# Optimization experiments

Hardware: AMD Instinct MI355X
Metric: run time of the kernel (lower is better)

## Reference

```python
import jax, jax.numpy as jnp
import numpy as np

N = 25000      # nodes
E = 400000     # edges (before self-loops)
D = 64         # input node feature dim
H = 4          # attention heads
C = 64         # out channels per head (concat=False -> head mean)
L = 3          # stacked layers
NEG_SLOPE = 0.2
EPS = 1e-5


def setup_inputs() -> dict:
    key = jax.random.key(0)
    ks = jax.random.split(key, 8)
    s = 0.1
    return {
        "x": jax.random.normal(ks[0], (N, D), jnp.float32),
        "edge_index": jax.random.randint(ks[1], (2, E), 0, N, dtype=jnp.int64),
        "Wl": jax.random.normal(ks[2], (L, H * C, D), jnp.float32) * s,
        "bl": jnp.zeros((L, H * C), jnp.float32),
        "Wr": jax.random.normal(ks[3], (L, H * C, D), jnp.float32) * s,
        "br": jnp.zeros((L, H * C), jnp.float32),
        "att": jax.random.normal(ks[4], (L, H, C), jnp.float32) * s,
        "conv_bias": jnp.zeros((L, C), jnp.float32),
        "gn_weight": jnp.ones((L, C), jnp.float32),
        "gn_scale": jnp.ones((L, C), jnp.float32),   # GraphNorm mean_scale (alpha)
        "gn_bias": jnp.zeros((L, C), jnp.float32),
    }


def _gat_forward(x, src, dst, Wl, bl, Wr, br, att, conv_bias,
                 gn_weight, gn_scale, gn_bias):
    n = x.shape[0]
    for i in range(L):
        # GATv2Conv (edge_attr=None, concat=False): separate source/target projections
        xl = (x @ Wl[i].T + bl[i]).reshape(n, H, C)  # [N,H,C]
        xr = (x @ Wr[i].T + br[i]).reshape(n, H, C)
        # per-edge attention logits: att . leaky_relu(xl[j] + xr[i])
        e = jax.nn.leaky_relu(xl[src] + xr[dst], NEG_SLOPE)      # [E',H,C]
        logits = jnp.einsum('ehc,hc->eh', e, att[i])             # [E',H]
        # segment softmax over incoming edges of each target node
        m = jax.ops.segment_max(logits, dst, num_segments=n)     # [N,H]
        a = jnp.exp(logits - m[dst])
        denom = jax.ops.segment_sum(a, dst, num_segments=n)      # [N,H]
        alpha = a / denom[dst]                                   # [E',H]
        # weighted scatter-add of source messages, mean over heads
        agg = jax.ops.segment_sum(xl[src] * alpha[:, :, None], dst,
                                  num_segments=n)                # [N,H,C]
        h = agg.mean(axis=1) + conv_bias[i]                      # [N,C]
        # GraphNorm (single graph): x - alpha*mean, scale by rstd
        mu = h.mean(axis=0)
        hc = h - gn_scale[i] * mu
        var = jnp.mean(hc * hc, axis=0)
        x = hc * jax.lax.rsqrt(var + EPS) * gn_weight[i] + gn_bias[i]
        # Dropout p=0 at eval -> identity
    return x


def reference(x, edge_index, Wl, bl, Wr, br, att, conv_bias,
              gn_weight, gn_scale, gn_bias):
    n = x.shape[0]
    loop = jnp.arange(n, dtype=edge_index.dtype)
    # PyG GATv2Conv adds self-loops by default
    src = jnp.concatenate([edge_index[0], loop])
    dst = jnp.concatenate([edge_index[1], loop])
    return _gat_forward(x, src, dst, Wl, bl, Wr, br, att, conv_bias,
                        gn_weight, gn_scale, gn_bias)
```

## Files before the change

### kernel.cpp

```cpp
#include <hip/hip_runtime.h>
#include <hip/hip_fp16.h>
#include <math.h>

#define HC   256
#define DD   64
#define CC   64
#define NLAY 3

#define RCAP    64
#define RCAP_SH 6

typedef _Float16 h2 __attribute__((ext_vector_type(2)));
typedef _Float16 h4 __attribute__((ext_vector_type(4)));
typedef _Float16 h8 __attribute__((ext_vector_type(8)));
typedef float    f4 __attribute__((ext_vector_type(4)));
typedef float    f2 __attribute__((ext_vector_type(2)));

#define XSTR 72
#define OSTR 276

__global__ __launch_bounds__(256) void zero_kernel(int* __restrict__ counts,
                                                   float* __restrict__ stats,
                                                   int n) {
    int i = blockIdx.x * 256 + threadIdx.x;
    if (i < n) counts[i] = 0;
    if (i < NLAY * 128) stats[i] = 0.f;
}

__global__ __launch_bounds__(256) void fill_kernel(const int* __restrict__ srcArr,
                                                   const int* __restrict__ dstArr,
                                                   int* __restrict__ counts,
                                                   int* __restrict__ csr_src,
                                                   int e, int n) {
    int i = blockIdx.x * 256 + threadIdx.x;
    if (i >= e + n) return;
    int s, d;
    if (i < e) { s = srcArr[i]; d = dstArr[i]; }
    else       { s = d = i - e; }
    int slot = atomicAdd(&counts[d], 1);
    if (slot < RCAP) csr_src[(d << RCAP_SH) + slot] = s;
}

__global__ __launch_bounds__(256) void proj_kernel(const float* __restrict__ x,
                                                   const float* __restrict__ Wl,
                                                   const float* __restrict__ bl,
                                                   const float* __restrict__ Wr,
                                                   const float* __restrict__ br,
                                                   __half* __restrict__ xl,
                                                   __half* __restrict__ xr, int n,
                                                   const float* __restrict__ stats,
                                                   const float* __restrict__ pgw,
                                                   const float* __restrict__ pgs,
                                                   const float* __restrict__ pgb) {
    __shared__ _Float16 xs[64 * XSTR];
    __shared__ _Float16 ws[256 * XSTR];
    __shared__ float nrm_a[64], nrm_b[64];
    const int t  = threadIdx.x;
    const int n0 = blockIdx.x * 64;

    if (t < 64) {
        float a = 1.f, b = 0.f;
        if (stats) {
            float inv_n = 1.0f / (float)n;
            float mu  = stats[t] * inv_n;
            float eh2 = stats[64 + t] * inv_n;
            float al  = pgs[t];
            float var = eh2 - 2.f * al * mu * mu + al * al * mu * mu;
            float rstd = rsqrtf(var + 1e-5f);
            a = pgw[t] * rstd;
            b = pgb[t] - al * mu * a;
        }
        nrm_a[t] = a; nrm_b[t] = b;
    }
    __syncthreads();

    {
        const float* xb = x + (size_t)n0 * DD;
        const int limit = (n - n0) * DD;
        #pragma unroll
        for (int it = 0; it < 4; ++it) {
            int f = (it * 256 + t) * 4;
            float4 v = make_float4(0.f, 0.f, 0.f, 0.f);
            if (f + 3 < limit) v = *(const float4*)(xb + f);
            else {
                float tmp[4] = {0.f, 0.f, 0.f, 0.f};
                for (int q = 0; q < 4; ++q) if (f + q < limit) tmp[q] = xb[f + q];
                v = make_float4(tmp[0], tmp[1], tmp[2], tmp[3]);
            }
            int d = f & 63;
            const float4 a4 = *(const float4*)&nrm_a[d];
            const float4 b4 = *(const float4*)&nrm_b[d];
            h4 hv;
            hv.x = (_Float16)fmaf(v.x, a4.x, b4.x);
            hv.y = (_Float16)fmaf(v.y, a4.y, b4.y);
            hv.z = (_Float16)fmaf(v.z, a4.z, b4.z);
            hv.w = (_Float16)fmaf(v.w, a4.w, b4.w);
            *(h4*)&xs[(f >> 6) * XSTR + d] = hv;
        }
    }

    const int w = t >> 6, lane = t & 63, m = lane & 15, q = lane >> 4;

    h8 A0, A1;
    f4 acc[16];

    #define STAGE_W(Wsel)                                                     \
    {                                                                         \
        _Pragma("unroll")                                                     \
        for (int it = 0; it < 16; ++it) {                                     \
            int f = (it * 256 + t) * 4;                                       \
            float4 v = *(const float4*)((Wsel) + f);                          \
            h4 hv = { (_Float16)v.x, (_Float16)v.y, (_Float16)v.z,            \
                      (_Float16)v.w };                                        \
            *(h4*)&ws[(f >> 6) * XSTR + (f & 63)] = hv;                       \
        }                                                                     \
    }

    #define MFMA_PASS()                                                       \
    {                                                                         \
        _Pragma("unroll")                                                     \
        for (int ct = 0; ct < 16; ++ct) {                                     \
            const _Float16* brow = ws + (ct * 16 + m) * XSTR + q * 8;         \
            const h8 B0 = *(const h8*)brow;                                   \
            const h8 B1 = *(const h8*)(brow + 32);                            \
            f4 c = {0.f, 0.f, 0.f, 0.f};                                      \
            c = __builtin_amdgcn_mfma_f32_16x16x32_f16(A0, B0, c, 0, 0, 0);   \
            c = __builtin_amdgcn_mfma_f32_16x16x32_f16(A1, B1, c, 0, 0, 0);   \
            acc[ct] = c;                                                      \
        }                                                                     \
    }

    #define EPILOGUE(bsel, osel)                                              \
    {                                                                         \
        _Pragma("unroll")                                                     \
        for (int ct = 0; ct < 16; ++ct) {                                     \
            int ch = ct * 16 + m;                                             \
            float bv = (bsel)[ch];                                            \
            _Pragma("unroll")                                                 \
            for (int r = 0; r < 4; ++r)                                       \
                ws[(w * 16 + q * 4 + r) * OSTR + ch] =                        \
                    (_Float16)(acc[ct][r] + bv);                              \
        }                                                                     \
        __syncthreads();                                                      \
        _Pragma("unroll")                                                     \
        for (int it = 0; it < 8; ++it) {                                      \
            int f   = (it * 256 + t) * 8;                                     \
            int row = f >> 8, ch = f & 255;                                   \
            if (n0 + row < n)                                                 \
                *(uint4*)((osel) + (size_t)(n0 + row) * HC + ch) =            \
                    *(const uint4*)&ws[row * OSTR + ch];                      \
        }                                                                     \
    }

    STAGE_W(Wl)
    __syncthreads();
    {
        const _Float16* arow = xs + (w * 16 + m) * XSTR + q * 8;
        A0 = *(const h8*)arow;
        A1 = *(const h8*)(arow + 32);
    }
    MFMA_PASS()
    __syncthreads();
    EPILOGUE(bl, xl)
    __syncthreads();

    STAGE_W(Wr)
    __syncthreads();
    MFMA_PASS()
    __syncthreads();
    EPILOGUE(br, xr)

    #undef STAGE_W
    #undef MFMA_PASS
    #undef EPILOGUE
}

__global__ __launch_bounds__(256) void attn_kernel(const __half* __restrict__ xl,
                                                   const __half* __restrict__ xr,
                                                   const float* __restrict__ att,
                                                   const float* __restrict__ conv_bias,
                                                   const int* __restrict__ counts,
                                                   const int* __restrict__ csr_src,
                                                   float* __restrict__ h_out, int n) {
    const int wave = threadIdx.x >> 6;
    const int l    = threadIdx.x & 63;
    const int v    = blockIdx.x * 4 + wave;
    if (v >= n) return;

    const int e2 = l >> 5;
    const int h  = (l >> 3) & 3;
    const int co = l & 7;
    const int choff = h * CC + co * 8;

    h2 xr2[4];
    *(uint4*)xr2 = *(const uint4*)(xr + (size_t)v * HC + choff);
    h2 at2[4];
    {
        const float* ap = att + choff;
        float4 a0 = *(const float4*)(ap);
        float4 a1 = *(const float4*)(ap + 4);
        at2[0] = (h2){(_Float16)a0.x, (_Float16)a0.y};
        at2[1] = (h2){(_Float16)a0.z, (_Float16)a0.w};
        at2[2] = (h2){(_Float16)a1.x, (_Float16)a1.y};
        at2[3] = (h2){(_Float16)a1.z, (_Float16)a1.w};
    }
    const _Float16 k02 = (_Float16)0.2f;

    const int rs = v << RCAP_SH;
    const int re = rs + counts[v];

    float s = 0.f;
    h2 acch[4];
    #pragma unroll
    for (int q = 0; q < 4; ++q) acch[q] = (h2){(_Float16)0.f, (_Float16)0.f};

    #define CLAMPI(i) (((i) < re) ? (i) : rs)

    uint4 r0 = *(const uint4*)(xl + (size_t)csr_src[CLAMPI(rs + e2)]     * HC + choff);
    uint4 r1 = *(const uint4*)(xl + (size_t)csr_src[CLAMPI(rs + 2 + e2)] * HC + choff);
    uint4 r2 = *(const uint4*)(xl + (size_t)csr_src[CLAMPI(rs + 4 + e2)] * HC + choff);
    int jnA = csr_src[CLAMPI(rs + 6 + e2)];
    int jnB = csr_src[CLAMPI(rs + 8 + e2)];
    int jnC = csr_src[CLAMPI(rs + 10 + e2)];

    #define STAGE(RBUF, JREG, VOFF, JOFF)                                 \
    {                                                                     \
        const uint4 cur = RBUF;                                           \
        RBUF = *(const uint4*)(xl + (size_t)JREG * HC + choff);           \
        JREG = csr_src[CLAMPI(k + JOFF + e2)];                            \
        const bool valid = (k + VOFF + e2) < re;                          \
        const h2* xh = (const h2*)&cur;                                   \
        h2 d2 = (h2){(_Float16)0.f, (_Float16)0.f};                      \
        _Pragma("unroll")                                                 \
        for (int q = 0; q < 4; ++q) {                                     \
            h2 tt = xh[q] + xr2[q];                                       \
            h2 lk = __builtin_elementwise_max(tt, tt * k02);              \
            d2 += lk * at2[q];                                            \
        }                                                                 \
        float p = (float)d2.x + (float)d2.y;                              \
        p += __shfl_xor(p, 1, 64);                                        \
        p += __shfl_xor(p, 2, 64);                                        \
        p += __shfl_xor(p, 4, 64);                                        \
        float pe = valid ? __expf(p) : 0.f;                               \
        s += pe;                                                          \
        const _Float16 peh = (_Float16)pe;                                \
        const h2 pe2 = (h2){peh, peh};                                    \
        _Pragma("unroll")                                                 \
        for (int q = 0; q < 4; ++q)                                       \
            acch[q] += pe2 * xh[q];                                       \
    }

    for (int k = rs; k < re; k += 6) {
        STAGE(r0, jnA, 0, 12)
        STAGE(r1, jnB, 2, 14)
        STAGE(r2, jnC, 4, 16)
    }
    #undef STAGE
    #undef CLAMPI

    s += __shfl_xor(s, 32, 64);
    const float inv = 1.f / s;
    float out8[8];
    #pragma unroll
    for (int q = 0; q < 8; ++q) {
        float av = (q & 1) ? (float)acch[q >> 1].y : (float)acch[q >> 1].x;
        float a = av + __shfl_xor(av, 32, 64);
        a *= inv;
        a += __shfl_xor(a, 8, 64);
        a += __shfl_xor(a, 16, 64);
        out8[q] = 0.25f * a;
    }
    if (l < 8) {
        const float4 cb0 = *(const float4*)(conv_bias + co * 8);
        const float4 cb1 = *(const float4*)(conv_bias + co * 8 + 4);
        float4 o0 = make_float4(out8[0] + cb0.x, out8[1] + cb0.y,
                                out8[2] + cb0.z, out8[3] + cb0.w);
        float4 o1 = make_float4(out8[4] + cb1.x, out8[5] + cb1.y,
                                out8[6] + cb1.z, out8[7] + cb1.w);
        float* op = h_out + (size_t)v * CC + co * 8;
        *(float4*)op       = o0;
        *(float4*)(op + 4) = o1;
    }
}

__global__ __launch_bounds__(256) void stats_kernel(const float* __restrict__ h,
                                                    float* __restrict__ stats, int n) {
    int t = threadIdx.x;
    int c = t & 63, r = t >> 6;
    float s = 0.f, s2 = 0.f;
    for (int node = blockIdx.x * 4 + r; node < n; node += gridDim.x * 4) {
        float v = h[node * CC + c];
        s += v; s2 += v * v;
    }
    __shared__ float l1[256], l2[256];
    l1[t] = s; l2[t] = s2;
    __syncthreads();
    if (t < 64) {
        s  = l1[t] + l1[64 + t] + l1[128 + t] + l1[192 + t];
        s2 = l2[t] + l2[64 + t] + l2[128 + t] + l2[192 + t];
        atomicAdd(&stats[c], s);
        atomicAdd(&stats[64 + c], s2);
    }
}

__global__ __launch_bounds__(256) void norm_kernel(const float* __restrict__ h,
                                                   const float* __restrict__ stats,
                                                   const float* __restrict__ gw,
                                                   const float* __restrict__ gs,
                                                   const float* __restrict__ gb,
                                                   float* __restrict__ out, int n) {
    __shared__ float na[64], nb[64];
    int t = threadIdx.x;
    if (t < 64) {
        float inv_n = 1.0f / (float)n;
        float mu  = stats[t] * inv_n;
        float eh2 = stats[64 + t] * inv_n;
        float a   = gs[t];
        float var = eh2 - 2.f * a * mu * mu + a * a * mu * mu;
        float rstd = rsqrtf(var + 1e-5f);
        na[t] = gw[t] * rstd;
        nb[t] = gb[t] - a * mu * gw[t] * rstd;
    }
    __syncthreads();
    int c = t & 63;
    float w = na[c], b = nb[c];
    int total = n * CC;
    for (int idx = blockIdx.x * 256 + t; idx < total; idx += gridDim.x * 256)
        out[idx] = fmaf(h[idx], w, b);
}

extern "C" void kernel_launch(void* const* d_in, const int* in_sizes, int n_in,
                              void* d_out, int out_size, void* d_ws, size_t ws_size,
                              hipStream_t stream) {
    const float* x0  = (const float*)d_in[0];
    const int*   ei  = (const int*)d_in[1];
    const float* Wl  = (const float*)d_in[2];
    const float* bl  = (const float*)d_in[3];
    const float* Wr  = (const float*)d_in[4];
    const float* br  = (const float*)d_in[5];
    const float* att = (const float*)d_in[6];
    const float* cb  = (const float*)d_in[7];
    const float* gw  = (const float*)d_in[8];
    const float* gs  = (const float*)d_in[9];
    const float* gb  = (const float*)d_in[10];

    const int n = in_sizes[0] / DD;
    const int e = in_sizes[1] / 2;
    const int* srcArr = ei;
    const int* dstArr = ei + e;

    char* w = (char*)d_ws;
    auto alloc = [&](size_t bytes) -> char* {
        char* p = w;
        w += (bytes + 255) & ~(size_t)255;
        return p;
    };
    __half* xl    = (__half*)alloc((size_t)n * HC * 2);
    __half* xr    = (__half*)alloc((size_t)n * HC * 2);
    float* hbuf   = (float*)alloc((size_t)n * CC * 4);
    int*   counts = (int*)  alloc((size_t)n * 4);
    int*   csr    = (int*)  alloc((size_t)n * RCAP * 4);
    float* stats  = (float*)alloc(NLAY * 128 * 4);

    const int tot = e + n;
    hipLaunchKernelGGL(zero_kernel,  dim3((n + 255) / 256),   dim3(256), 0, stream,
                       counts, stats, n);
    hipLaunchKernelGGL(fill_kernel,  dim3((tot + 255) / 256), dim3(256), 0, stream,
                       srcArr, dstArr, counts, csr, e, n);

    for (int L = 0; L < NLAY; ++L) {
        const float* xin = (L == 0) ? x0 : hbuf;
        const int Lp = (L == 0) ? 0 : L - 1;
        const float* st = (L == 0) ? nullptr : stats + (size_t)Lp * 128;
        hipLaunchKernelGGL(proj_kernel, dim3((n + 63) / 64), dim3(256), 0, stream,
                           xin, Wl + (size_t)L * HC * DD, bl + L * HC,
                           Wr + (size_t)L * HC * DD, br + L * HC, xl, xr, n,
                           st, gw + Lp * CC, gs + Lp * CC, gb + Lp * CC);
        hipLaunchKernelGGL(attn_kernel, dim3((n + 3) / 4), dim3(256), 0, stream,
                           xl, xr, att + L * HC, cb + L * CC, counts, csr, hbuf, n);
        hipLaunchKernelGGL(stats_kernel, dim3(128), dim3(256), 0, stream,
                           hbuf, stats + (size_t)L * 128, n);
    }
    hipLaunchKernelGGL(norm_kernel, dim3(512), dim3(256), 0, stream,
                       hbuf, stats + (size_t)(NLAY - 1) * 128, gw + (NLAY - 1) * CC,
                       gs + (NLAY - 1) * CC, gb + (NLAY - 1) * CC,
                       (float*)d_out, n);
}
```

Before: 301.2 us.

## Fuse GraphNorm statistics into attention epilogue with bucketed atomic partials

The separate per-layer stats kernel is removed. The attention kernel now reduces each block's output sum and sum of squares in shared memory. It then atomically adds them into one of 64 partial-sum buckets, which spreads the contention. The projection and norm kernels sum the 64 buckets before computing mean and variance. This avoids one extra kernel launch and a full re-read of the hidden buffer per layer. The cost is many extra float atomics, a block-wide barrier in the attention kernel, and a small reduction at the start of every consumer block.

```diff
diff --git a/kernel.cpp b/kernel.cpp
--- a/kernel.cpp
+++ b/kernel.cpp
@@ -9,6 +9,8 @@
 
 #define RCAP    64
 #define RCAP_SH 6
+
+#define NBKT 64
 
 typedef _Float16 h2 __attribute__((ext_vector_type(2)));
 typedef _Float16 h4 __attribute__((ext_vector_type(4)));
@@ -20,11 +22,11 @@
 #define OSTR 276
 
 __global__ __launch_bounds__(256) void zero_kernel(int* __restrict__ counts,
-                                                   float* __restrict__ stats,
+                                                   float* __restrict__ spart,
                                                    int n) {
     int i = blockIdx.x * 256 + threadIdx.x;
     if (i < n) counts[i] = 0;
-    if (i < NLAY * 128) stats[i] = 0.f;
+    if (i < NLAY * NBKT * 128) spart[i] = 0.f;
 }
 
 __global__ __launch_bounds__(256) void fill_kernel(const int* __restrict__ srcArr,
@@ -48,22 +50,30 @@
                                                    const float* __restrict__ br,
                                                    __half* __restrict__ xl,
                                                    __half* __restrict__ xr, int n,
-                                                   const float* __restrict__ stats,
+                                                   const float* __restrict__ spart,
                                                    const float* __restrict__ pgw,
                                                    const float* __restrict__ pgs,
                                                    const float* __restrict__ pgb) {
     __shared__ _Float16 xs[64 * XSTR];
     __shared__ _Float16 ws[256 * XSTR];
     __shared__ float nrm_a[64], nrm_b[64];
+    __shared__ float sred[128];
     const int t  = threadIdx.x;
     const int n0 = blockIdx.x * 64;
 
+    if (spart && t < 128) {
+        float a = 0.f;
+        #pragma unroll 8
+        for (int r = 0; r < NBKT; ++r) a += spart[r * 128 + t];
+        sred[t] = a;
+    }
+    __syncthreads();
     if (t < 64) {
         float a = 1.f, b = 0.f;
-        if (stats) {
+        if (spart) {
             float inv_n = 1.0f / (float)n;
-            float mu  = stats[t] * inv_n;
-            float eh2 = stats[64 + t] * inv_n;
+            float mu  = sred[t] * inv_n;
+            float eh2 = sred[64 + t] * inv_n;
             float al  = pgs[t];
             float var = eh2 - 2.f * al * mu * mu + al * al * mu * mu;
             float rstd = rsqrtf(var + 1e-5f);
@@ -181,140 +191,151 @@
                                                    const float* __restrict__ conv_bias,
                                                    const int* __restrict__ counts,
                                                    const int* __restrict__ csr_src,
-                                                   float* __restrict__ h_out, int n) {
+                                                   float* __restrict__ h_out,
+                                                   float* __restrict__ spart, int n) {
+    __shared__ float ps[4][64], ps2[4][64];
     const int wave = threadIdx.x >> 6;
     const int l    = threadIdx.x & 63;
     const int v    = blockIdx.x * 4 + wave;
-    if (v >= n) return;
+    const bool active = (v < n);
 
     const int e2 = l >> 5;
     const int h  = (l >> 3) & 3;
     const int co = l & 7;
     const int choff = h * CC + co * 8;
 
-    h2 xr2[4];
-    *(uint4*)xr2 = *(const uint4*)(xr + (size_t)v * HC + choff);
-    h2 at2[4];
-    {
-        const float* ap = att + choff;
-        float4 a0 = *(const float4*)(ap);
-        float4 a1 = *(const float4*)(ap + 4);
-        at2[0] = (h2){(_Float16)a0.x, (_Float16)a0.y};
-        at2[1] = (h2){(_Float16)a0.z, (_Float16)a0.w};
-        at2[2] = (h2){(_Float16)a1.x, (_Float16)a1.y};
-        at2[3] = (h2){(_Float16)a1.z, (_Float16)a1.w};
-    }
-    const _Float16 k02 = (_Float16)0.2f;
-
-    const int rs = v << RCAP_SH;
-    const int re = rs + counts[v];
-
-    float s = 0.f;
-    h2 acch[4];
-    #pragma unroll
-    for (int q = 0; q < 4; ++q) acch[q] = (h2){(_Float16)0.f, (_Float16)0.f};
-
-    #define CLAMPI(i) (((i) < re) ? (i) : rs)
-
-    uint4 r0 = *(const uint4*)(xl + (size_t)csr_src[CLAMPI(rs + e2)]     * HC + choff);
-    uint4 r1 = *(const uint4*)(xl + (size_t)csr_src[CLAMPI(rs + 2 + e2)] * HC + choff);
-    uint4 r2 = *(const uint4*)(xl + (size_t)csr_src[CLAMPI(rs + 4 + e2)] * HC + choff);
-    int jnA = csr_src[CLAMPI(rs + 6 + e2)];
-    int jnB = csr_src[CLAMPI(rs + 8 + e2)];
-    int jnC = csr_src[CLAMPI(rs + 10 + e2)];
-
-    #define STAGE(RBUF, JREG, VOFF, JOFF)                                 \
-    {                                                                     \
-        const uint4 cur = RBUF;                                           \
-        RBUF = *(const uint4*)(xl + (size_t)JREG * HC + choff);           \
-        JREG = csr_src[CLAMPI(k + JOFF + e2)];                            \
-        const bool valid = (k + VOFF + e2) < re;                          \
-        const h2* xh = (const h2*)&cur;                                   \
-        h2 d2 = (h2){(_Float16)0.f, (_Float16)0.f};                      \
-        _Pragma("unroll")                                                 \
-        for (int q = 0; q < 4; ++q) {                                     \
-            h2 tt = xh[q] + xr2[q];                                       \
-            h2 lk = __builtin_elementwise_max(tt, tt * k02);              \
-            d2 += lk * at2[q];                                            \
-        }                                                                 \
-        float p = (float)d2.x + (float)d2.y;                              \
-        p += __shfl_xor(p, 1, 64);                                        \
-        p += __shfl_xor(p, 2, 64);                                        \
-        p += __shfl_xor(p, 4, 64);                                        \
-        float pe = valid ? __expf(p) : 0.f;                               \
-        s += pe;                                                          \
-        const _Float16 peh = (_Float16)pe;                                \
-        const h2 pe2 = (h2){peh, peh};                                    \
-        _Pragma("unroll")                                                 \
-        for (int q = 0; q < 4; ++q)                                       \
-            acch[q] += pe2 * xh[q];                                       \
-    }
-
-    for (int k = rs; k < re; k += 6) {
-        STAGE(r0, jnA, 0, 12)
-        STAGE(r1, jnB, 2, 14)
-        STAGE(r2, jnC, 4, 16)
-    }
-    #undef STAGE
-    #undef CLAMPI
-
-    s += __shfl_xor(s, 32, 64);
-    const float inv = 1.f / s;
-    float out8[8];
-    #pragma unroll
-    for (int q = 0; q < 8; ++q) {
-        float av = (q & 1) ? (float)acch[q >> 1].y : (float)acch[q >> 1].x;
-        float a = av + __shfl_xor(av, 32, 64);
-        a *= inv;
-        a += __shfl_xor(a, 8, 64);
-        a += __shfl_xor(a, 16, 64);
-        out8[q] = 0.25f * a;
-    }
-    if (l < 8) {
-        const float4 cb0 = *(const float4*)(conv_bias + co * 8);
-        const float4 cb1 = *(const float4*)(conv_bias + co * 8 + 4);
-        float4 o0 = make_float4(out8[0] + cb0.x, out8[1] + cb0.y,
-                                out8[2] + cb0.z, out8[3] + cb0.w);
-        float4 o1 = make_float4(out8[4] + cb1.x, out8[5] + cb1.y,
-                                out8[6] + cb1.z, out8[7] + cb1.w);
-        float* op = h_out + (size_t)v * CC + co * 8;
-        *(float4*)op       = o0;
-        *(float4*)(op + 4) = o1;
-    }
-}
-
-__global__ __launch_bounds__(256) void stats_kernel(const float* __restrict__ h,
-                                                    float* __restrict__ stats, int n) {
-    int t = threadIdx.x;
-    int c = t & 63, r = t >> 6;
-    float s = 0.f, s2 = 0.f;
-    for (int node = blockIdx.x * 4 + r; node < n; node += gridDim.x * 4) {
-        float v = h[node * CC + c];
-        s += v; s2 += v * v;
-    }
-    __shared__ float l1[256], l2[256];
-    l1[t] = s; l2[t] = s2;
-    __syncthreads();
-    if (t < 64) {
-        s  = l1[t] + l1[64 + t] + l1[128 + t] + l1[192 + t];
-        s2 = l2[t] + l2[64 + t] + l2[128 + t] + l2[192 + t];
-        atomicAdd(&stats[c], s);
-        atomicAdd(&stats[64 + c], s2);
+    if (active) {
+        h2 xr2[4];
+        *(uint4*)xr2 = *(const uint4*)(xr + (size_t)v * HC + choff);
+        h2 at2[4];
+        {
+            const float* ap = att + choff;
+            float4 a0 = *(const float4*)(ap);
+            float4 a1 = *(const float4*)(ap + 4);
+            at2[0] = (h2){(_Float16)a0.x, (_Float16)a0.y};
+            at2[1] = (h2){(_Float16)a0.z, (_Float16)a0.w};
+            at2[2] = (h2){(_Float16)a1.x, (_Float16)a1.y};
+            at2[3] = (h2){(_Float16)a1.z, (_Float16)a1.w};
+        }
+        const _Float16 k02 = (_Float16)0.2f;
+
+        const int rs = v << RCAP_SH;
+        const int re = rs + counts[v];
+
+        float s = 0.f;
+        h2 acch[4];
+        #pragma unroll
+        for (int q = 0; q < 4; ++q) acch[q] = (h2){(_Float16)0.f, (_Float16)0.f};
+
+        #define CLAMPI(i) (((i) < re) ? (i) : rs)
+
+        uint4 r0 = *(const uint4*)(xl + (size_t)csr_src[CLAMPI(rs + e2)]     * HC + choff);
+        uint4 r1 = *(const uint4*)(xl + (size_t)csr_src[CLAMPI(rs + 2 + e2)] * HC + choff);
+        uint4 r2 = *(const uint4*)(xl + (size_t)csr_src[CLAMPI(rs + 4 + e2)] * HC + choff);
+        int jnA = csr_src[CLAMPI(rs + 6 + e2)];
+        int jnB = csr_src[CLAMPI(rs + 8 + e2)];
+        int jnC = csr_src[CLAMPI(rs + 10 + e2)];
+
+        #define STAGE(RBUF, JREG, VOFF, JOFF)                                 \
+        {                                                                     \
+            const uint4 cur = RBUF;                                           \
+            RBUF = *(const uint4*)(xl + (size_t)JREG * HC + choff);           \
+            JREG = csr_src[CLAMPI(k + JOFF + e2)];                            \
+            const bool valid = (k + VOFF + e2) < re;                          \
+            const h2* xh = (const h2*)&cur;                                   \
+            h2 d2 = (h2){(_Float16)0.f, (_Float16)0.f};                      \
+            _Pragma("unroll")                                                 \
+            for (int q = 0; q < 4; ++q) {                                     \
+                h2 tt = xh[q] + xr2[q];                                       \
+                h2 lk = __builtin_elementwise_max(tt, tt * k02);              \
+                d2 += lk * at2[q];                                            \
+            }                                                                 \
+            float p = (float)d2.x + (float)d2.y;                              \
+            p += __shfl_xor(p, 1, 64);                                        \
+            p += __shfl_xor(p, 2, 64);                                        \
+            p += __shfl_xor(p, 4, 64);                                        \
+            float pe = valid ? __expf(p) : 0.f;                               \
+            s += pe;                                                          \
+            const _Float16 peh = (_Float16)pe;                                \
+            const h2 pe2 = (h2){peh, peh};                                    \
+            _Pragma("unroll")                                                 \
+            for (int q = 0; q < 4; ++q)                                       \
+                acch[q] += pe2 * xh[q];                                       \
+        }
+
+        for (int k = rs; k < re; k += 6) {
+            STAGE(r0, jnA, 0, 12)
+            STAGE(r1, jnB, 2, 14)
+            STAGE(r2, jnC, 4, 16)
+        }
+        #undef STAGE
+        #undef CLAMPI
+
+        s += __shfl_xor(s, 32, 64);
+        const float inv = 1.f / s;
+        float out8[8];
+        #pragma unroll
+        for (int q = 0; q < 8; ++q) {
+            float av = (q & 1) ? (float)acch[q >> 1].y : (float)acch[q >> 1].x;
+            float a = av + __shfl_xor(av, 32, 64);
+            a *= inv;
+            a += __shfl_xor(a, 8, 64);
+            a += __shfl_xor(a, 16, 64);
+            out8[q] = 0.25f * a;
+        }
+        if (l < 8) {
+            const float4 cb0 = *(const float4*)(conv_bias + co * 8);
+            const float4 cb1 = *(const float4*)(conv_bias + co * 8 + 4);
+            float4 o0 = make_float4(out8[0] + cb0.x, out8[1] + cb0.y,
+                                    out8[2] + cb0.z, out8[3] + cb0.w);
+            float4 o1 = make_float4(out8[4] + cb1.x, out8[5] + cb1.y,
+                                    out8[6] + cb1.z, out8[7] + cb1.w);
+            float* op = h_out + (size_t)v * CC + co * 8;
+            *(float4*)op       = o0;
+            *(float4*)(op + 4) = o1;
+            ps [wave][co * 8 + 0] = o0.x;  ps2[wave][co * 8 + 0] = o0.x * o0.x;
+            ps [wave][co * 8 + 1] = o0.y;  ps2[wave][co * 8 + 1] = o0.y * o0.y;
+            ps [wave][co * 8 + 2] = o0.z;  ps2[wave][co * 8 + 2] = o0.z * o0.z;
+            ps [wave][co * 8 + 3] = o0.w;  ps2[wave][co * 8 + 3] = o0.w * o0.w;
+            ps [wave][co * 8 + 4] = o1.x;  ps2[wave][co * 8 + 4] = o1.x * o1.x;
+            ps [wave][co * 8 + 5] = o1.y;  ps2[wave][co * 8 + 5] = o1.y * o1.y;
+            ps [wave][co * 8 + 6] = o1.z;  ps2[wave][co * 8 + 6] = o1.z * o1.z;
+            ps [wave][co * 8 + 7] = o1.w;  ps2[wave][co * 8 + 7] = o1.w * o1.w;
+        }
+    } else if (l < 8) {
+        #pragma unroll
+        for (int q = 0; q < 8; ++q) { ps[wave][l * 8 + q] = 0.f; ps2[wave][l * 8 + q] = 0.f; }
+    }
+    __syncthreads();
+    if (threadIdx.x < 128) {
+        const int c = threadIdx.x & 63;
+        const float (*src)[64] = (threadIdx.x < 64) ? ps : ps2;
+        float sum = src[0][c] + src[1][c] + src[2][c] + src[3][c];
+        atomicAdd(&spart[(blockIdx.x & (NBKT - 1)) * 128 +
+                         ((threadIdx.x < 64) ? c : 64 + c)], sum);
     }
 }
 
 __global__ __launch_bounds__(256) void norm_kernel(const float* __restrict__ h,
-                                                   const float* __restrict__ stats,
+                                                   const float* __restrict__ spart,
                                                    const float* __restrict__ gw,
                                                    const float* __restrict__ gs,
                                                    const float* __restrict__ gb,
                                                    float* __restrict__ out, int n) {
+    __shared__ float sred[128];
     __shared__ float na[64], nb[64];
     int t = threadIdx.x;
+    if (t < 128) {
+        float a = 0.f;
+        #pragma unroll 8
+        for (int r = 0; r < NBKT; ++r) a += spart[r * 128 + t];
+        sred[t] = a;
+    }
+    __syncthreads();
     if (t < 64) {
         float inv_n = 1.0f / (float)n;
-        float mu  = stats[t] * inv_n;
-        float eh2 = stats[64 + t] * inv_n;
+        float mu  = sred[t] * inv_n;
+        float eh2 = sred[64 + t] * inv_n;
         float a   = gs[t];
         float var = eh2 - 2.f * a * mu * mu + a * a * mu * mu;
         float rstd = rsqrtf(var + 1e-5f);
@@ -360,29 +381,28 @@
     float* hbuf   = (float*)alloc((size_t)n * CC * 4);
     int*   counts = (int*)  alloc((size_t)n * 4);
     int*   csr    = (int*)  alloc((size_t)n * RCAP * 4);
-    float* stats  = (float*)alloc(NLAY * 128 * 4);
+    float* spart  = (float*)alloc((size_t)NLAY * NBKT * 128 * 4);
 
     const int tot = e + n;
     hipLaunchKernelGGL(zero_kernel,  dim3((n + 255) / 256),   dim3(256), 0, stream,
-                       counts, stats, n);
+                       counts, spart, n);
     hipLaunchKernelGGL(fill_kernel,  dim3((tot + 255) / 256), dim3(256), 0, stream,
                        srcArr, dstArr, counts, csr, e, n);
 
     for (int L = 0; L < NLAY; ++L) {
         const float* xin = (L == 0) ? x0 : hbuf;
         const int Lp = (L == 0) ? 0 : L - 1;
-        const float* st = (L == 0) ? nullptr : stats + (size_t)Lp * 128;
+        const float* sp = (L == 0) ? nullptr : spart + (size_t)Lp * NBKT * 128;
         hipLaunchKernelGGL(proj_kernel, dim3((n + 63) / 64), dim3(256), 0, stream,
                            xin, Wl + (size_t)L * HC * DD, bl + L * HC,
                            Wr + (size_t)L * HC * DD, br + L * HC, xl, xr, n,
-                           st, gw + Lp * CC, gs + Lp * CC, gb + Lp * CC);
+                           sp, gw + Lp * CC, gs + Lp * CC, gb + Lp * CC);
         hipLaunchKernelGGL(attn_kernel, dim3((n + 3) / 4), dim3(256), 0, stream,
-                           xl, xr, att + L * HC, cb + L * CC, counts, csr, hbuf, n);
-        hipLaunchKernelGGL(stats_kernel, dim3(128), dim3(256), 0, stream,
-                           hbuf, stats + (size_t)L * 128, n);
+                           xl, xr, att + L * HC, cb + L * CC, counts, csr, hbuf,
+                           spart + (size_t)L * NBKT * 128, n);
     }
     hipLaunchKernelGGL(norm_kernel, dim3(512), dim3(256), 0, stream,
-                       hbuf, stats + (size_t)(NLAY - 1) * 128, gw + (NLAY - 1) * CC,
-                       gs + (NLAY - 1) * CC, gb + (NLAY - 1) * CC,
-                       (float*)d_out, n);
-}
+                       hbuf, spart + (size_t)(NLAY - 1) * NBKT * 128,
+                       gw + (NLAY - 1) * CC, gs + (NLAY - 1) * CC,
+                       gb + (NLAY - 1) * CC, (float*)d_out, n);
+}
```

Result: faster. 283.8 us (-5.8%).
